# Performance work log

Measured on AMD Instinct MI355X. Metric: run time of the kernel, lower is better.

Reference implementation:

```python
import jax, jax.numpy as jnp
import numpy as np

VAR_XY = 0.1  # SSD encoding variances
VAR_WH = 0.2


def _iou(truths, priors):
    # truths [G,4], priors [P,4] in corner form (x1,y1,x2,y2) -> [G,P]
    lt = jnp.maximum(truths[:, None, :2], priors[None, :, :2])
    rb = jnp.minimum(truths[:, None, 2:], priors[None, :, 2:])
    wh = jnp.clip(rb - lt, 0.0, None)
    inter = wh[..., 0] * wh[..., 1]
    area_t = (truths[:, 2] - truths[:, 0]) * (truths[:, 3] - truths[:, 1])
    area_p = (priors[:, 2] - priors[:, 0]) * (priors[:, 3] - priors[:, 1])
    return inter / (area_t[:, None] + area_p[None, :] - inter)


def _encode(truths, matched):
    # truths [G,1,4], matched priors [G,k,4], corner form -> SSD offsets [G,k,4]
    p_cxcy = (matched[..., :2] + matched[..., 2:]) * 0.5
    p_wh = matched[..., 2:] - matched[..., :2]
    g_cxcy = (truths[..., :2] + truths[..., 2:]) * 0.5
    g_wh = truths[..., 2:] - truths[..., :2]
    off_xy = (g_cxcy - p_cxcy) / (VAR_XY * p_wh)
    off_wh = jnp.log(g_wh / p_wh) / VAR_WH
    return jnp.concatenate([off_xy, off_wh], axis=-1)


def setup_inputs() -> dict:
    key = jax.random.key(0)
    k1, k2, k3, k4 = jax.random.split(key, 4)
    B, P, G = 16, 32768, 128
    # priors: valid corner-form boxes built from centers + sizes
    p_c = jax.random.uniform(k1, (B, P, 2), minval=0.1, maxval=0.9)
    p_s = jax.random.uniform(k2, (B, P, 2), minval=0.02, maxval=0.3)
    priors = jnp.concatenate([p_c - p_s * 0.5, p_c + p_s * 0.5], axis=-1)
    rpn_rois = jnp.stack([priors, priors], axis=1)  # [B,2,P,4]; channel 1 used
    # GT boxes, valid corner form
    t_c = jax.random.uniform(k3, (B, G, 2), minval=0.1, maxval=0.9)
    t_s = jax.random.uniform(k4, (B, G, 2), minval=0.05, maxval=0.4)
    targets = jnp.concatenate([t_c - t_s * 0.5, t_c + t_s * 0.5], axis=-1)
    return {"rpn_rois": rpn_rois, "targets": targets, "expand_num": 4}


def reference(rpn_rois, targets, expand_num):
    defaults = rpn_rois[:, 1]  # [B,P,4]

    def per_image(truths, priors):
        ious = _iou(truths, priors)                      # [G,P]
        _, idx = jax.lax.top_k(ious, expand_num)         # [G,k] best priors per GT
        matched = priors[idx]                            # [G,k,4]
        off = _encode(truths[:, None, :], matched)       # [G,k,4]
        return off.reshape(-1, 4)                        # [G*k,4]

    return jax.vmap(per_image)(targets, defaults)        # [B, G*k, 4]
```

## Files before the change

kernel.cpp:

```cpp
#include <hip/hip_runtime.h>

#define B 16
#define P 32768
#define NG 128
#define KTOP 4
#define NBX 32
#define NBY 32
#define NBB (NBX * NBY)
#define SUB 16
#define SUBP (P / SUB)
typedef unsigned long long u64;
typedef unsigned int u32;

__device__ __forceinline__ int bkt(float v) {
    int k = (int)((v + 0.08f) * 32.0f);
    return k < 0 ? 0 : (k > 31 ? 31 : k);
}

__device__ __forceinline__ void ceu(u64 &x, u64 &y) {
    u64 a = x, b = y; bool gt = a > b;
    x = gt ? a : b;  y = gt ? b : a;
}
__device__ __forceinline__ void cef(float &x, float &y) {
    float h = fmaxf(x, y), l = fminf(x, y); x = h; y = l;
}

#define INS4(x, a0, a1, a2, a3)                                   \
    {                                                             \
        bool g0 = (x) > a0, g1 = (x) > a1, g2 = (x) > a2, g3 = (x) > a3; \
        u64 n3 = g2 ? a2 : (g3 ? (x) : a3);                       \
        u64 n2 = g1 ? a1 : (g2 ? (x) : a2);                       \
        u64 n1 = g0 ? a0 : (g1 ? (x) : a1);                       \
        u64 n0 = g0 ? (x) : a0;                                   \
        a0 = n0; a1 = n1; a2 = n2; a3 = n3;                       \
    }

#define IOUKEY(q, oi, dst)                                        \
    {                                                             \
        float ap = ((q).z - (q).x) * ((q).w - (q).y);             \
        float ltx = fmaxf(t0, (q).x), lty = fmaxf(t1, (q).y);     \
        float rbx = fminf(t2, (q).z), rby = fminf(t3, (q).w);     \
        float wx = fmaxf(rbx - ltx, 0.0f);                        \
        float wy = fmaxf(rby - lty, 0.0f);                        \
        float inter = wx * wy;                                    \
        float iou = inter / ((areaT + ap) - inter);               \
        dst = ((u64)__float_as_uint(iou) << 32) | (u32)(~(oi));   \
    }

__global__ __launch_bounds__(256)
void k_hist(const float* __restrict__ rois, u32* __restrict__ cnt, float* __restrict__ whm)
{
    const int b = blockIdx.x >> 4, sub = blockIdx.x & 15;
    const int tid = threadIdx.x;
    __shared__ u32 h[NBB];
    __shared__ float red[8];
    for (int j = tid; j < NBB; j += 256) h[j] = 0;
    __syncthreads();

    const float4* __restrict__ pv = (const float4*)(rois + ((size_t)(2 * b + 1)) * P * 4);
    float wmax = 0.f, hmax = 0.f;
    #pragma unroll
    for (int it = 0; it < SUBP / 256; ++it) {
        float4 q = pv[sub * SUBP + it * 256 + tid];
        atomicAdd(&h[bkt(q.x) * NBY + bkt(q.y)], 1u);
        wmax = fmaxf(wmax, q.z - q.x);
        hmax = fmaxf(hmax, q.w - q.y);
    }
    #pragma unroll
    for (int d = 32; d >= 1; d >>= 1) {
        wmax = fmaxf(wmax, __shfl_down(wmax, d, 64));
        hmax = fmaxf(hmax, __shfl_down(hmax, d, 64));
    }
    if ((tid & 63) == 0) { red[(tid >> 6) * 2] = wmax; red[(tid >> 6) * 2 + 1] = hmax; }
    __syncthreads();
    for (int j = tid; j < NBB; j += 256) cnt[(size_t)blockIdx.x * NBB + j] = h[j];
    if (tid == 0) {
        whm[blockIdx.x * 2 + 0] = fmaxf(fmaxf(red[0], red[2]), fmaxf(red[4], red[6]));
        whm[blockIdx.x * 2 + 1] = fmaxf(fmaxf(red[1], red[3]), fmaxf(red[5], red[7]));
    }
}

__global__ __launch_bounds__(256)
void k_scat(const float* __restrict__ rois, const u32* __restrict__ cnt,
            float4* __restrict__ sbox, u32* __restrict__ sidx, u32* __restrict__ off)
{
    const int b = blockIdx.x >> 4, sub = blockIdx.x & 15;
    const int tid = threadIdx.x;
    const int lane = tid & 63, wv = tid >> 6;
    __shared__ u32 cur[NBB];
    __shared__ u32 wpart[4];

    u32 bintot[4] = {0, 0, 0, 0};
    u32 below[4]  = {0, 0, 0, 0};
    #pragma unroll
    for (int k = 0; k < SUB; ++k) {
        #pragma unroll
        for (int m = 0; m < 4; ++m) {
            u32 v = cnt[(size_t)(b * SUB + k) * NBB + 4 * tid + m];
            bintot[m] += v;
            if (k < sub) below[m] += v;
        }
    }
    u32 s_local = bintot[0] + bintot[1] + bintot[2] + bintot[3];
    u32 incl = s_local;
    #pragma unroll
    for (int d = 1; d < 64; d <<= 1) {
        u32 v = __shfl_up(incl, d, 64);
        if (lane >= d) incl += v;
    }
    if (lane == 63) wpart[wv] = incl;
    __syncthreads();
    u32 wbase = 0;
    #pragma unroll
    for (int w = 0; w < 4; ++w) if (w < wv) wbase += wpart[w];

    u32 run = wbase + incl - s_local;
    #pragma unroll
    for (int m = 0; m < 4; ++m) {
        cur[4 * tid + m] = run + below[m];
        if (sub == 0) off[b * (NBB + 1) + 4 * tid + m] = run;
        run += bintot[m];
    }
    if (sub == 0 && tid == 0) off[b * (NBB + 1) + NBB] = P;
    __syncthreads();

    const float4* __restrict__ pv = (const float4*)(rois + ((size_t)(2 * b + 1)) * P * 4);
    #pragma unroll
    for (int it = 0; it < SUBP / 256; ++it) {
        int i = sub * SUBP + it * 256 + tid;
        float4 q = pv[i];
        u32 slot = atomicAdd(&cur[bkt(q.x) * NBY + bkt(q.y)], 1u);
        sbox[(size_t)b * P + slot] = q;
        sidx[(size_t)b * P + slot] = (u32)i;
    }
}

__global__ __launch_bounds__(256, 4)
void k_main(const float* __restrict__ rois, const float* __restrict__ targets,
            const float4* __restrict__ sbox, const u32* __restrict__ sidx,
            const u32* __restrict__ off, const float* __restrict__ whm,
            float* __restrict__ out)
{
    #pragma clang fp contract(off)

    const int blk = blockIdx.x;
    const int b   = ((blk & 7) << 1) | ((blk >> 3) & 1);
    const int g   = blk >> 4;
    const int tid = threadIdx.x;
    const int lane = tid & 63, wv = tid >> 6;

    const float* tp = targets + ((size_t)(b * NG + g)) * 4;
    const float t0 = tp[0], t1 = tp[1], t2 = tp[2], t3 = tp[3];
    const float areaT = (t2 - t0) * (t3 - t1);
    const float gw = t2 - t0, gh = t3 - t1;

    const float4* __restrict__ boxb = sbox + (size_t)b * P;
    const u32*    __restrict__ idxb = sidx + (size_t)b * P;
    const u32*    __restrict__ offb = off + b * (NBB + 1);

    __shared__ float sf[4][4];
    __shared__ u64   sm[4][4];
    __shared__ int   seg_lo[NBX], seg_hi[NBX];

    float w0 = -1.f, w1 = -1.f, w2 = -1.f, w3 = -1.f;
    #pragma unroll
    for (int it = 0; it < 8; ++it) {
        float4 q = boxb[(it * 4 + wv) * (P / 32) + lane];
        float ap = (q.z - q.x) * (q.w - q.y);
        float ltx = fmaxf(t0, q.x), lty = fmaxf(t1, q.y);
        float rbx = fminf(t2, q.z), rby = fminf(t3, q.w);
        float wx = fmaxf(rbx - ltx, 0.0f);
        float wy = fmaxf(rby - lty, 0.0f);
        float inter = wx * wy;
        float iou = inter / ((areaT + ap) - inter);
        float x = iou, hh;
        hh = fmaxf(w0, x); x = fminf(w0, x); w0 = hh;
        hh = fmaxf(w1, x); x = fminf(w1, x); w1 = hh;
        hh = fmaxf(w2, x); x = fminf(w2, x); w2 = hh;
        w3 = fmaxf(w3, x);
    }
    #pragma unroll
    for (int d = 32; d >= 1; d >>= 1) {
        float n0 = __shfl_down(w0, d, 64);
        float n1 = __shfl_down(w1, d, 64);
        float n2 = __shfl_down(w2, d, 64);
        float n3 = __shfl_down(w3, d, 64);
        cef(w0, n3); cef(w1, n2); cef(w2, n1); cef(w3, n0);
        cef(w0, w2); cef(w1, w3); cef(w0, w1); cef(w2, w3);
    }
    if (lane == 0) { sf[wv][0] = w0; sf[wv][1] = w1; sf[wv][2] = w2; sf[wv][3] = w3; }
    __syncthreads();

    if (wv == 0) {
        float m0 = -1.f, m1 = -1.f, m2 = -1.f, m3 = -1.f;
        #pragma unroll
        for (int j = 0; j < 16; ++j) {
            float x = sf[j >> 2][j & 3], hh;
            hh = fmaxf(m0, x); x = fminf(m0, x); m0 = hh;
            hh = fmaxf(m1, x); x = fminf(m1, x); m1 = hh;
            hh = fmaxf(m2, x); x = fminf(m2, x); m2 = hh;
            m3 = fmaxf(m3, x);
        }
        float wm = 0.f, hm = 0.f;
        #pragma unroll
        for (int k = 0; k < SUB; ++k) {
            wm = fmaxf(wm, whm[(b * SUB + k) * 2 + 0]);
            hm = fmaxf(hm, whm[(b * SUB + k) * 2 + 1]);
        }
        float lb = m3 * 0.999f;
        int bxlo = 0, bxhi = 31, bylo = 0, byhi = 31;
        if (lb > 1e-6f) {
            bxlo = bkt(t0 + lb * gw - wm - 1e-5f);
            bxhi = bkt(t2 - lb * gw + 1e-5f);
            bylo = bkt(t1 + lb * gh - hm - 1e-5f);
            byhi = bkt(t3 - lb * gh + 1e-5f);
        }
        if (lane < NBX) {
            bool inx = (lane >= bxlo) && (lane <= bxhi);
            int lo = (int)offb[lane * NBY + bylo];
            int hi = (int)offb[lane * NBY + byhi + 1];
            seg_lo[lane] = lo;
            seg_hi[lane] = inx ? hi : lo;
        }
    }
    __syncthreads();

    u64 a0 = 0, a1 = 0, a2 = 0, a3 = 0;
    u64 c0 = 0, c1 = 0, c2 = 0, c3 = 0;
    for (int s = wv; s < NBX; s += 4) {
        const int lo = seg_lo[s];
        const int n = seg_hi[s] - lo;
        const float4* __restrict__ bp = boxb + lo;
        const u32*    __restrict__ ip = idxb + lo;

        float4 qa0 = {0,0,0,0}, qb0 = {0,0,0,0}, qa1 = {0,0,0,0}, qb1 = {0,0,0,0};
        u32 oa0 = 0, ob0 = 0, oa1 = 0, ob1 = 0;
        if (lane < n)       { qa0 = bp[lane];       oa0 = ip[lane]; }
        if (lane + 64 < n)  { qb0 = bp[lane + 64];  ob0 = ip[lane + 64]; }
        if (lane + 128 < n) { qa1 = bp[lane + 128]; oa1 = ip[lane + 128]; }
        if (lane + 192 < n) { qb1 = bp[lane + 192]; ob1 = ip[lane + 192]; }

        for (int base = 0; base < n; base += 128) {
            float4 qa2 = qa1, qb2 = qb1; u32 oa2 = oa1, ob2 = ob1;
            const int ja = base + 256 + lane, jb = base + 320 + lane;
            if (ja < n) { qa2 = bp[ja]; oa2 = ip[ja]; }
            if (jb < n) { qb2 = bp[jb]; ob2 = ip[jb]; }

            if (base + lane < n) {
                u64 x; IOUKEY(qa0, oa0, x);
                INS4(x, a0, a1, a2, a3);
            }
            if (base + 64 + lane < n) {
                u64 x; IOUKEY(qb0, ob0, x);
                INS4(x, c0, c1, c2, c3);
            }
            qa0 = qa1; oa0 = oa1; qb0 = qb1; ob0 = ob1;
            qa1 = qa2; oa1 = oa2; qb1 = qb2; ob1 = ob2;
        }
    }
    ceu(a0, c3); ceu(a1, c2); ceu(a2, c1); ceu(a3, c0);
    ceu(a0, a2); ceu(a1, a3); ceu(a0, a1); ceu(a2, a3);

    #pragma unroll
    for (int d = 32; d >= 1; d >>= 1) {
        u64 n0 = __shfl_down(a0, d, 64);
        u64 n1 = __shfl_down(a1, d, 64);
        u64 n2 = __shfl_down(a2, d, 64);
        u64 n3 = __shfl_down(a3, d, 64);
        ceu(a0, n3); ceu(a1, n2); ceu(a2, n1); ceu(a3, n0);
        ceu(a0, a2); ceu(a1, a3); ceu(a0, a1); ceu(a2, a3);
    }
    if (lane == 0) { sm[wv][0] = a0; sm[wv][1] = a1; sm[wv][2] = a2; sm[wv][3] = a3; }
    __syncthreads();

    if (tid == 0) {
        u64 f0 = 0, f1 = 0, f2 = 0, f3 = 0;
        #pragma unroll
        for (int j = 0; j < 16; ++j) {
            u64 x = sm[j >> 2][j & 3];
            INS4(x, f0, f1, f2, f3);
        }
        const float gcx = (t0 + t2) * 0.5f;
        const float gcy = (t1 + t3) * 0.5f;
        const float4* __restrict__ pv =
            (const float4*)(rois + ((size_t)(2 * b + 1)) * P * 4);
        float4* __restrict__ o4 = (float4*)out;

        u64 ks[KTOP] = {f0, f1, f2, f3};
        #pragma unroll
        for (int k = 0; k < KTOP; ++k) {
            int idx = (int)(~(u32)ks[k]) & (P - 1);
            float4 q = pv[idx];
            float pcx = (q.x + q.z) * 0.5f;
            float pcy = (q.y + q.w) * 0.5f;
            float pw  = q.z - q.x;
            float ph  = q.w - q.y;
            float4 r;
            r.x = (gcx - pcx) / (0.1f * pw);
            r.y = (gcy - pcy) / (0.1f * ph);
            r.z = logf(gw / pw) / 0.2f;
            r.w = logf(gh / ph) / 0.2f;
            o4[((size_t)(b * NG + g)) * KTOP + k] = r;
        }
    }
}

extern "C" void kernel_launch(void* const* d_in, const int* in_sizes, int n_in,
                              void* d_out, int out_size, void* d_ws, size_t ws_size,
                              hipStream_t stream) {
    const float* rois    = (const float*)d_in[0];
    const float* targets = (const float*)d_in[1];
    float* out = (float*)d_out;

    char* w = (char*)d_ws;
    float4* sbox = (float4*)(w);
    u32*    sidx = (u32*)  (w + (size_t)B * P * 16);
    u32*    cnt  = (u32*)  (w + (size_t)B * P * 20);
    u32*    off  = (u32*)  (w + (size_t)B * P * 24);
    float*  whm  = (float*)(w + (size_t)B * P * 24 + 66560);

    k_hist<<<dim3(B * SUB), dim3(256), 0, stream>>>(rois, cnt, whm);
    k_scat<<<dim3(B * SUB), dim3(256), 0, stream>>>(rois, cnt, sbox, sidx, off);
    k_main<<<dim3(B * NG),  dim3(256), 0, stream>>>(rois, targets, sbox, sidx, off, whm, out);
}
```

Before: 121.5 us.

## Split each GT's bucket scan across two blocks and merge top-4 in encode kernel

```diff
diff --git a/kernel.cpp b/kernel.cpp
--- a/kernel.cpp
+++ b/kernel.cpp
@@ -136,16 +136,19 @@
 }
 
 __global__ __launch_bounds__(256, 4)
-void k_main(const float* __restrict__ rois, const float* __restrict__ targets,
+void k_main(const float* __restrict__ targets,
             const float4* __restrict__ sbox, const u32* __restrict__ sidx,
             const u32* __restrict__ off, const float* __restrict__ whm,
-            float* __restrict__ out)
+            u64* __restrict__ cand)
 {
     #pragma clang fp contract(off)
 
     const int blk = blockIdx.x;
-    const int b   = ((blk & 7) << 1) | ((blk >> 3) & 1);
-    const int g   = blk >> 4;
+    const int b    = ((blk & 7) << 1) | ((blk >> 3) & 1);
+    const int r    = blk >> 4;
+    if (r >= 2 * NG) return;
+    const int half = r & 1;
+    const int g    = r >> 1;
     const int tid = threadIdx.x;
     const int lane = tid & 63, wv = tid >> 6;
 
@@ -164,8 +167,8 @@
 
     float w0 = -1.f, w1 = -1.f, w2 = -1.f, w3 = -1.f;
     #pragma unroll
-    for (int it = 0; it < 8; ++it) {
-        float4 q = boxb[(it * 4 + wv) * (P / 32) + lane];
+    for (int it = 0; it < 4; ++it) {
+        float4 q = boxb[(it * 4 + wv) * (P / 16) + lane];
         float ap = (q.z - q.x) * (q.w - q.y);
         float ltx = fmaxf(t0, q.x), lty = fmaxf(t1, q.y);
         float rbx = fminf(t2, q.z), rby = fminf(t3, q.w);
@@ -227,7 +230,8 @@
 
     u64 a0 = 0, a1 = 0, a2 = 0, a3 = 0;
     u64 c0 = 0, c1 = 0, c2 = 0, c3 = 0;
-    for (int s = wv; s < NBX; s += 4) {
+    for (int k = 0; k < 4; ++k) {
+        const int s = half + 2 * wv + 8 * k;
         const int lo = seg_lo[s];
         const int n = seg_hi[s] - lo;
         const float4* __restrict__ bp = boxb + lo;
@@ -280,28 +284,56 @@
             u64 x = sm[j >> 2][j & 3];
             INS4(x, f0, f1, f2, f3);
         }
-        const float gcx = (t0 + t2) * 0.5f;
-        const float gcy = (t1 + t3) * 0.5f;
-        const float4* __restrict__ pv =
-            (const float4*)(rois + ((size_t)(2 * b + 1)) * P * 4);
-        float4* __restrict__ o4 = (float4*)out;
-
-        u64 ks[KTOP] = {f0, f1, f2, f3};
-        #pragma unroll
-        for (int k = 0; k < KTOP; ++k) {
-            int idx = (int)(~(u32)ks[k]) & (P - 1);
-            float4 q = pv[idx];
-            float pcx = (q.x + q.z) * 0.5f;
-            float pcy = (q.y + q.w) * 0.5f;
-            float pw  = q.z - q.x;
-            float ph  = q.w - q.y;
-            float4 r;
-            r.x = (gcx - pcx) / (0.1f * pw);
-            r.y = (gcy - pcy) / (0.1f * ph);
-            r.z = logf(gw / pw) / 0.2f;
-            r.w = logf(gh / ph) / 0.2f;
-            o4[((size_t)(b * NG + g)) * KTOP + k] = r;
-        }
+        const int tg = b * NG + g;
+        u64* my = cand + (size_t)tg * 8 + half * 4;
+        my[0] = f0; my[1] = f1; my[2] = f2; my[3] = f3;
+    }
+}
+
+__global__ __launch_bounds__(256)
+void k_enc(const float* __restrict__ rois, const float* __restrict__ targets,
+           const u64* __restrict__ cand, float* __restrict__ out, int ntruth)
+{
+    #pragma clang fp contract(off)
+
+    const int tg = blockIdx.x * 256 + threadIdx.x;
+    if (tg >= ntruth) return;
+    const int b = tg >> 7;
+
+    const u64* c = cand + (size_t)tg * 8;
+    u64 f0 = 0, f1 = 0, f2 = 0, f3 = 0;
+    #pragma unroll
+    for (int j = 0; j < 8; ++j) {
+        u64 x = c[j];
+        INS4(x, f0, f1, f2, f3);
+    }
+
+    const float* tp = targets + (size_t)tg * 4;
+    const float t0 = tp[0], t1 = tp[1], t2 = tp[2], t3 = tp[3];
+    const float gcx = (t0 + t2) * 0.5f;
+    const float gcy = (t1 + t3) * 0.5f;
+    const float gw  = t2 - t0;
+    const float gh  = t3 - t1;
+
+    const float4* __restrict__ pv =
+        (const float4*)(rois + ((size_t)(2 * b + 1)) * P * 4);
+    float4* __restrict__ o4 = (float4*)out;
+
+    u64 ks[KTOP] = {f0, f1, f2, f3};
+    #pragma unroll
+    for (int k = 0; k < KTOP; ++k) {
+        int idx = (int)(~(u32)ks[k]) & (P - 1);
+        float4 q = pv[idx];
+        float pcx = (q.x + q.z) * 0.5f;
+        float pcy = (q.y + q.w) * 0.5f;
+        float pw  = q.z - q.x;
+        float ph  = q.w - q.y;
+        float4 r;
+        r.x = (gcx - pcx) / (0.1f * pw);
+        r.y = (gcy - pcy) / (0.1f * ph);
+        r.z = logf(gw / pw) / 0.2f;
+        r.w = logf(gh / ph) / 0.2f;
+        o4[(size_t)tg * KTOP + k] = r;
     }
 }
 
@@ -318,8 +350,12 @@
     u32*    cnt  = (u32*)  (w + (size_t)B * P * 20);
     u32*    off  = (u32*)  (w + (size_t)B * P * 24);
     float*  whm  = (float*)(w + (size_t)B * P * 24 + 66560);
+    u64*    cand = (u64*)  (w + (size_t)B * P * 24 + 66560 + 2048);
+
+    const int ntruth = B * NG;
 
     k_hist<<<dim3(B * SUB), dim3(256), 0, stream>>>(rois, cnt, whm);
     k_scat<<<dim3(B * SUB), dim3(256), 0, stream>>>(rois, cnt, sbox, sidx, off);
-    k_main<<<dim3(B * NG),  dim3(256), 0, stream>>>(rois, targets, sbox, sidx, off, whm, out);
-}
+    k_main<<<dim3(2 * B * NG), dim3(256), 0, stream>>>(targets, sbox, sidx, off, whm, cand);
+    k_enc <<<dim3((ntruth + 255) / 256), dim3(256), 0, stream>>>(rois, targets, cand, out, ntruth);
+}
```

Result: slower. 132.7 us (+9.2%).
